# Kernel optimization log

Hardware: AMD Instinct MI355X
Metric: run time of the kernel (lower is better)

Reference implementation:

```python
import jax, jax.numpy as jnp
import numpy as np

EMBED_DIM = 1024
LAMBDA_INIT = 0.8
EPS = 1e-5


def setup_inputs() -> dict:
    key = jax.random.key(0)
    ks = jax.random.split(key, 8)
    D = EMBED_DIM
    x = jax.random.normal(ks[0], (4, 2048, D), dtype=jnp.float32)
    # torch Linear weight [out, in]; we store transposed [in, out] for x @ W
    s = 1.0 / np.sqrt(D)
    w_q12 = jax.random.uniform(ks[1], (D, 2 * D), jnp.float32, -s, s)
    w_k12 = jax.random.uniform(ks[2], (D, 2 * D), jnp.float32, -s, s)
    w_v = jax.random.uniform(ks[3], (D, D), jnp.float32, -s, s)
    lambda_q1 = 0.1 * jax.random.normal(ks[4], (D,), jnp.float32)
    lambda_k1 = 0.1 * jax.random.normal(ks[5], (D,), jnp.float32)
    lambda_q2 = 0.1 * jax.random.normal(ks[6], (D,), jnp.float32)
    lambda_k2 = 0.1 * jax.random.normal(ks[7], (D,), jnp.float32)
    return {"x": x, "w_q12": w_q12, "w_k12": w_k12, "w_v": w_v,
            "lambda_q1": lambda_q1, "lambda_k1": lambda_k1,
            "lambda_q2": lambda_q2, "lambda_k2": lambda_k2}


def reference(x, w_q12, w_k12, w_v, lambda_q1, lambda_k1, lambda_q2, lambda_k2):
    D = x.shape[-1]
    scale = D ** (-0.25)
    q12 = jnp.einsum('bsd,de->bse', x, w_q12)
    k12 = jnp.einsum('bsd,de->bse', x, w_k12)
    q1, q2 = jnp.split(q12, 2, axis=-1)
    k1, k2 = jnp.split(k12, 2, axis=-1)
    v = jnp.einsum('bsd,de->bse', x, w_v)
    attn1 = jnp.einsum('bqd,bkd->bqk', q1, k1) * scale
    attn2 = jnp.einsum('bqd,bkd->bqk', q2, k2) * scale
    lam1 = jnp.exp(jnp.sum(lambda_q1 * lambda_k1))
    lam2 = jnp.exp(jnp.sum(lambda_q2 * lambda_k2))
    lam_full = lam1 - lam2 + LAMBDA_INIT
    diff = jax.nn.softmax(attn1, axis=-1) - lam_full * jax.nn.softmax(attn2, axis=-1)
    out = jnp.einsum('bqk,bkd->bqd', diff, v)
    # RMSNorm (no affine), then scale by (1 - lambda_init)
    rms = jnp.sqrt(jnp.mean(out * out, axis=-1, keepdims=True) + EPS)
    return (out / rms) * (1.0 - LAMBDA_INIT)
```

## Files before the change

kernel.cpp:

```cpp
#include <hip/hip_runtime.h>

typedef float f32x4 __attribute__((ext_vector_type(4)));
typedef _Float16 h16x8 __attribute__((ext_vector_type(8)));
typedef _Float16 h16x4 __attribute__((ext_vector_type(4)));

#define GLOAD_LDS16(gp, lp) __builtin_amdgcn_global_load_lds(               \
    (const __attribute__((address_space(1))) void*)(gp),                    \
    (__attribute__((address_space(3))) void*)(lp), 16, 0, 0)

#define BARX do { __builtin_amdgcn_s_barrier(); asm volatile("" ::: "memory"); } while (0)
#define VMW(N) asm volatile("s_waitcnt vmcnt(" #N ")" ::: "memory")

__global__ __launch_bounds__(256) void cast_x(const float* __restrict__ x,
                                              _Float16* __restrict__ xh) {
  long i = (long)blockIdx.x * 256 + threadIdx.x;
  f32x4 a = *(const f32x4*)(x + i * 8);
  f32x4 b = *(const f32x4*)(x + i * 8 + 4);
  h16x8 h;
  h[0] = (_Float16)a[0]; h[1] = (_Float16)a[1];
  h[2] = (_Float16)a[2]; h[3] = (_Float16)a[3];
  h[4] = (_Float16)b[0]; h[5] = (_Float16)b[1];
  h[6] = (_Float16)b[2]; h[7] = (_Float16)b[3];
  *(h16x8*)(xh + i * 8) = h;
}

__global__ __launch_bounds__(256) void tcw(const float* __restrict__ in,
                                           _Float16* __restrict__ out,
                                           int Kd, int Nd, float scale) {
  __shared__ float tile[64][65];
  const int t = threadIdx.x;
  const int k0 = blockIdx.y * 64, n0 = blockIdx.x * 64;
  const int tr = t >> 4, tc = (t & 15) * 4;
#pragma unroll
  for (int i = 0; i < 4; ++i) {
    int r = i * 16 + tr;
    f32x4 a = *(const f32x4*)(in + (long)(k0 + r) * Nd + n0 + tc);
    tile[r][tc + 0] = a[0]; tile[r][tc + 1] = a[1];
    tile[r][tc + 2] = a[2]; tile[r][tc + 3] = a[3];
  }
  __syncthreads();
#pragma unroll
  for (int i = 0; i < 4; ++i) {
    int r = i * 16 + tr;
    h16x4 h;
#pragma unroll
    for (int q = 0; q < 4; ++q) h[q] = (_Float16)(tile[tc + q][r] * scale);
    *(h16x4*)(out + (long)(n0 + r) * Kd + k0 + tc) = h;
  }
}

__global__ __launch_bounds__(256) void trans16(const _Float16* __restrict__ in,
                                               _Float16* __restrict__ out,
                                               int R, int Cd, long ibatch, long obatch) {
  __shared__ _Float16 tile[64][72];
  in += (long)blockIdx.z * ibatch;
  out += (long)blockIdx.z * obatch;
  const int t = threadIdx.x;
  const int r0 = blockIdx.y * 64, c0 = blockIdx.x * 64;
  const int tr = t >> 3, tc8 = (t & 7) * 8;
#pragma unroll
  for (int i = 0; i < 2; ++i) {
    int r = i * 32 + tr;
    h16x8 a = *(const h16x8*)(in + (long)(r0 + r) * Cd + c0 + tc8);
    *(h16x8*)(&tile[r][tc8]) = a;
  }
  __syncthreads();
#pragma unroll
  for (int i = 0; i < 2; ++i) {
    int r = i * 32 + tr;
    h16x8 h;
#pragma unroll
    for (int q = 0; q < 8; ++q) h[q] = tile[tc8 + q][r];
    *(h16x8*)(out + (long)(c0 + r) * R + r0 + tc8) = h;
  }
}

__global__ __launch_bounds__(1024) void lambda_k(const float* __restrict__ lq1,
                                                 const float* __restrict__ lk1,
                                                 const float* __restrict__ lq2,
                                                 const float* __restrict__ lk2,
                                                 float* __restrict__ lam) {
  __shared__ float sh1[16], sh2[16];
  const int t = threadIdx.x;
  float p1 = lq1[t] * lk1[t];
  float p2 = lq2[t] * lk2[t];
#pragma unroll
  for (int off = 1; off < 64; off <<= 1) {
    p1 += __shfl_xor(p1, off);
    p2 += __shfl_xor(p2, off);
  }
  if ((t & 63) == 0) { sh1[t >> 6] = p1; sh2[t >> 6] = p2; }
  __syncthreads();
  if (t == 0) {
    float s1 = 0.f, s2 = 0.f;
    for (int i = 0; i < 16; ++i) { s1 += sh1[i]; s2 += sh2[i]; }
    lam[0] = __expf(s1) - __expf(s2) + 0.8f;
  }
}

template <typename CT>
__global__ __launch_bounds__(256, 2) void gemmv(
    const _Float16* __restrict__ A, const _Float16* __restrict__ B,
    CT* __restrict__ C, int K, int lda, int ldb, int ldc,
    long abatch, long bbatch, long cbatch, long a2, long c2, int natt,
    int nbx, int nby) {
  __shared__ _Float16 As[3][256 * 32];
  __shared__ _Float16 Bs[3][128 * 32];

  const int nwg = gridDim.x;
  const int orig = blockIdx.x;
  const int qd = nwg >> 3, rm = nwg & 7;
  const int xcd = orig & 7, sub = orig >> 3;
  const int wgid = (xcd < rm ? xcd * (qd + 1) : rm * (qd + 1) + (xcd - rm) * qd) + sub;

  const int z = wgid / (nbx * nby);
  const int rem = wgid - z * nbx * nby;
  const int by = rem / nbx;
  const int bx = rem - by * nbx;
  const int att = z % natt;
  const int bz = z / natt;

  const int t = threadIdx.x;
  const int lane = t & 63, wv = t >> 6;
  const int wm = wv >> 1, wn = wv & 1;
  const int lg = lane >> 4, l15 = lane & 15;

  const _Float16* Ab = A + (long)bz * abatch + (long)att * a2 + (long)(by * 256) * lda;
  const _Float16* Bb = B + (long)bz * bbatch + (long)att * a2 + (long)(bx * 128) * ldb;

  auto stage = [&](int slot, int S) {
    const long ko = (long)S * 32;
#pragma unroll
    for (int j = 0; j < 4; ++j) {
      const int e = t + j * 256;
      const int r = e >> 2;
      const int gs = ((e & 3) - (r >> 1)) & 3;
      GLOAD_LDS16(Ab + (long)r * lda + ko + gs * 8, &As[slot][e * 8]);
    }
#pragma unroll
    for (int j = 0; j < 2; ++j) {
      const int e = t + j * 256;
      const int r = e >> 2;
      const int gs = ((e & 3) - (r >> 1)) & 3;
      GLOAD_LDS16(Bb + (long)r * ldb + ko + gs * 8, &Bs[slot][e * 8]);
    }
  };

  int offA[8], offB[4];
#pragma unroll
  for (int m = 0; m < 8; ++m) {
    const int r = wm * 128 + m * 16 + l15;
    offA[m] = (r * 4 + ((lg + (r >> 1)) & 3)) * 8;
  }
#pragma unroll
  for (int n = 0; n < 4; ++n) {
    const int r = wn * 64 + n * 16 + l15;
    offB[n] = (r * 4 + ((lg + (r >> 1)) & 3)) * 8;
  }

  f32x4 acc[8][4] = {};
  const int NS = K >> 5;

  stage(0, 0); stage(1, 1);
  int cur = 0, nx2 = 2;

  for (int S = 0; S < NS; ++S) {
    if (S == NS - 1) VMW(0);
    else VMW(6);
    BARX;

    if (S + 2 < NS) stage(nx2, S + 2);

    const _Float16* Ap = &As[cur][0];
    const _Float16* Bp = &Bs[cur][0];
    h16x8 a[8], b[4];
#pragma unroll
    for (int m = 0; m < 8; ++m) a[m] = *(const h16x8*)(Ap + offA[m]);
#pragma unroll
    for (int n = 0; n < 4; ++n) b[n] = *(const h16x8*)(Bp + offB[n]);
    __builtin_amdgcn_s_setprio(1);
#pragma unroll
    for (int m = 0; m < 8; ++m)
#pragma unroll
      for (int n = 0; n < 4; ++n)
        acc[m][n] = __builtin_amdgcn_mfma_f32_16x16x32_f16(a[m], b[n], acc[m][n], 0, 0, 0);
    __builtin_amdgcn_s_setprio(0);

    cur = (cur == 2) ? 0 : cur + 1;
    nx2 = (nx2 == 2) ? 0 : nx2 + 1;
  }

  CT* Cb = C + (long)bz * cbatch + (long)att * c2;
  const int crow0 = by * 256 + wm * 128;
  const int ccol0 = bx * 128 + wn * 64;
#pragma unroll
  for (int m = 0; m < 8; ++m)
#pragma unroll
    for (int n = 0; n < 4; ++n)
#pragma unroll
      for (int j = 0; j < 4; ++j)
        Cb[(long)(crow0 + m * 16 + lg * 4 + j) * ldc + ccol0 + n * 16 + l15] =
            (CT)acc[m][n][j];
}

__global__ __launch_bounds__(256) void softmax_diff(const _Float16* __restrict__ S1,
                                                    const _Float16* __restrict__ S2,
                                                    _Float16* __restrict__ D,
                                                    const float* __restrict__ lamp) {
  const long row = (long)blockIdx.x * 4 + (threadIdx.x >> 6);
  const int lane = threadIdx.x & 63;
  const float lam = *lamp;
  const _Float16* s1 = S1 + row * 2048;
  const _Float16* s2 = S2 + row * 2048;
  float v1[32], v2[32];
  float m1 = -3e38f, m2 = -3e38f;
#pragma unroll
  for (int j = 0; j < 4; ++j) {
    h16x8 a = ((const h16x8*)s1)[j * 64 + lane];
    h16x8 b = ((const h16x8*)s2)[j * 64 + lane];
#pragma unroll
    for (int q = 0; q < 8; ++q) {
      v1[j * 8 + q] = (float)a[q]; v2[j * 8 + q] = (float)b[q];
      m1 = fmaxf(m1, v1[j * 8 + q]); m2 = fmaxf(m2, v2[j * 8 + q]);
    }
  }
#pragma unroll
  for (int off = 1; off < 64; off <<= 1) {
    m1 = fmaxf(m1, __shfl_xor(m1, off));
    m2 = fmaxf(m2, __shfl_xor(m2, off));
  }
  float l1 = 0.f, l2 = 0.f;
#pragma unroll
  for (int e = 0; e < 32; ++e) {
    v1[e] = __expf(v1[e] - m1); l1 += v1[e];
    v2[e] = __expf(v2[e] - m2); l2 += v2[e];
  }
#pragma unroll
  for (int off = 1; off < 64; off <<= 1) {
    l1 += __shfl_xor(l1, off);
    l2 += __shfl_xor(l2, off);
  }
  const float r1 = 1.f / l1, r2 = lam / l2;
  _Float16* d = D + row * 2048;
#pragma unroll
  for (int j = 0; j < 4; ++j) {
    h16x8 h;
#pragma unroll
    for (int q = 0; q < 8; ++q)
      h[q] = (_Float16)(v1[j * 8 + q] * r1 - v2[j * 8 + q] * r2);
    ((h16x8*)d)[j * 64 + lane] = h;
  }
}

__global__ __launch_bounds__(256) void rmsnorm(const _Float16* __restrict__ O,
                                               float* __restrict__ out) {
  const long row = (long)blockIdx.x * 4 + (threadIdx.x >> 6);
  const int lane = threadIdx.x & 63;
  const _Float16* o = O + row * 1024;
  h16x8 a = ((const h16x8*)o)[lane];
  h16x8 b = ((const h16x8*)o)[64 + lane];
  float xa[8], xb[8];
  float ss = 0.f;
#pragma unroll
  for (int q = 0; q < 8; ++q) {
    xa[q] = (float)a[q]; xb[q] = (float)b[q];
    ss += xa[q] * xa[q] + xb[q] * xb[q];
  }
#pragma unroll
  for (int off = 1; off < 64; off <<= 1) ss += __shfl_xor(ss, off);
  const float s = 0.2f * rsqrtf(ss * (1.f / 1024.f) + 1e-5f);
  float* po = out + row * 1024;
  f32x4 r;
#pragma unroll
  for (int q = 0; q < 4; ++q) r[q] = xa[q] * s;
  *(f32x4*)(po + lane * 8) = r;
#pragma unroll
  for (int q = 0; q < 4; ++q) r[q] = xa[4 + q] * s;
  *(f32x4*)(po + lane * 8 + 4) = r;
#pragma unroll
  for (int q = 0; q < 4; ++q) r[q] = xb[q] * s;
  *(f32x4*)(po + 512 + lane * 8) = r;
#pragma unroll
  for (int q = 0; q < 4; ++q) r[q] = xb[4 + q] * s;
  *(f32x4*)(po + 512 + lane * 8 + 4) = r;
}

extern "C" void kernel_launch(void* const* d_in, const int* in_sizes, int n_in,
                              void* d_out, int out_size, void* d_ws, size_t ws_size,
                              hipStream_t stream) {
  const float* x   = (const float*)d_in[0];
  const float* wq  = (const float*)d_in[1];
  const float* wk  = (const float*)d_in[2];
  const float* wv  = (const float*)d_in[3];
  const float* lq1 = (const float*)d_in[4];
  const float* lk1 = (const float*)d_in[5];
  const float* lq2 = (const float*)d_in[6];
  const float* lk2 = (const float*)d_in[7];
  float* out = (float*)d_out;

  const size_t MB = 1ull << 20;
  char* ws = (char*)d_ws;
  _Float16* xh   = (_Float16*)(ws + 0);
  _Float16* Wp   = (_Float16*)(ws + 16 * MB);
  _Float16* qkv  = (_Float16*)(ws + 26 * MB);
  _Float16* vt   = (_Float16*)(ws + 106 * MB);
  _Float16* S1   = (_Float16*)(ws + 122 * MB);
  _Float16* S2   = (_Float16*)(ws + 154 * MB);
  float*    lam  = (float*)(ws + 186 * MB);
  _Float16* diff = (_Float16*)(ws + 26 * MB);
  _Float16* opre = (_Float16*)(ws + 58 * MB);

  const float scale = 0.17677669529663689f;

  cast_x<<<4096, 256, 0, stream>>>(x, xh);
  tcw<<<dim3(32, 16), 256, 0, stream>>>(wq, Wp, 1024, 2048, scale);
  tcw<<<dim3(32, 16), 256, 0, stream>>>(wk, Wp + 2048l * 1024, 1024, 2048, 1.0f);
  tcw<<<dim3(16, 16), 256, 0, stream>>>(wv, Wp + 4096l * 1024, 1024, 1024, 1.0f);
  lambda_k<<<1, 1024, 0, stream>>>(lq1, lk1, lq2, lk2, lam);

  gemmv<_Float16><<<1280, 256, 0, stream>>>(xh, Wp, qkv, 1024, 1024, 1024, 5120,
                                            0, 0, 0, 0, 0, 1, 40, 32);

  trans16<<<dim3(16, 32, 4), 256, 0, stream>>>(qkv + 4096, vt, 2048, 5120,
                                               2048l * 5120, 1024l * 2048);

  gemmv<_Float16><<<1024, 256, 0, stream>>>(qkv, qkv + 2048, S1, 1024, 5120, 5120, 2048,
                                            2048l * 5120, 2048l * 5120, 2048l * 2048,
                                            1024, 16777216l, 2, 16, 8);

  softmax_diff<<<2048, 256, 0, stream>>>(S1, S2, diff, lam);

  gemmv<_Float16><<<256, 256, 0, stream>>>(diff, vt, opre, 2048, 2048, 2048, 1024,
                                           2048l * 2048, 1024l * 2048, 2048l * 1024,
                                           0, 0, 1, 8, 8);

  rmsnorm<<<2048, 256, 0, stream>>>(opre, out);
}
```

Measured before the change: 312.8 us.

## Replace GEMM with 8-wave 256x256 tile kernel using ping-pong sub-tile schedule

Replaces the 4-wave 256x128 triple-buffered GEMM with an 8-wave kernel using 256x256 (or 256x128) tiles, K-step 64, and double-buffered half-tiles. The loop interleaves LDS fragment reads, async global-to-LDS loads and four MFMA quadrants separated by barriers, and uses an XOR swizzle. It aims to raise arithmetic intensity per workgroup and hide load latency behind MFMA work. In exchange it adds many barriers and a higher register load, and it halves the grid for the QKV and score GEMMs, which may lower occupancy.

```diff
diff --git a/kernel.cpp b/kernel.cpp
--- a/kernel.cpp
+++ b/kernel.cpp
@@ -98,20 +98,23 @@
   }
 }
 
-template <typename CT>
-__global__ __launch_bounds__(256, 2) void gemmv(
+template <int NREP, typename CT>
+__global__ __launch_bounds__(512, 2) void g8(
     const _Float16* __restrict__ A, const _Float16* __restrict__ B,
     CT* __restrict__ C, int K, int lda, int ldb, int ldc,
     long abatch, long bbatch, long cbatch, long a2, long c2, int natt,
     int nbx, int nby) {
-  __shared__ _Float16 As[3][256 * 32];
-  __shared__ _Float16 Bs[3][128 * 32];
+  constexpr int BN = NREP * 64;
+  constexpr int BNH = BN / 2;
+  constexpr int NH = NREP / 2;
+  __shared__ _Float16 As[2][2][128 * 64];
+  __shared__ _Float16 Bs[2][2][BNH * 64];
 
   const int nwg = gridDim.x;
   const int orig = blockIdx.x;
   const int qd = nwg >> 3, rm = nwg & 7;
-  const int xcd = orig & 7, sub = orig >> 3;
-  const int wgid = (xcd < rm ? xcd * (qd + 1) : rm * (qd + 1) + (xcd - rm) * qd) + sub;
+  const int xcd = orig & 7, sub_ = orig >> 3;
+  const int wgid = (xcd < rm ? xcd * (qd + 1) : rm * (qd + 1) + (xcd - rm) * qd) + sub_;
 
   const int z = wgid / (nbx * nby);
   const int rem = wgid - z * nbx * nby;
@@ -122,85 +125,133 @@
 
   const int t = threadIdx.x;
   const int lane = t & 63, wv = t >> 6;
-  const int wm = wv >> 1, wn = wv & 1;
+  const int wm = wv >> 2, wn = wv & 3;
   const int lg = lane >> 4, l15 = lane & 15;
 
   const _Float16* Ab = A + (long)bz * abatch + (long)att * a2 + (long)(by * 256) * lda;
-  const _Float16* Bb = B + (long)bz * bbatch + (long)att * a2 + (long)(bx * 128) * ldb;
-
-  auto stage = [&](int slot, int S) {
-    const long ko = (long)S * 32;
+  const _Float16* Bb = B + (long)bz * bbatch + (long)att * a2 + (long)(bx * BN) * ldb;
+
+  auto stgA = [&](int T, int s) {
+    const int db = T & 1;
+#pragma unroll
+    for (int j = 0; j < 2; ++j) {
+      const int c = t + j * 512;
+      const int ru = c >> 3, p = c & 7;
+      const int gs = p ^ (ru & 7);
+      const int grow = (ru < 64) ? (s * 64 + ru) : (128 + s * 64 + (ru - 64));
+      GLOAD_LDS16(Ab + (long)grow * lda + T * 64 + gs * 8, &As[db][s][c * 8]);
+    }
+  };
+  auto stgB = [&](int T, int s) {
+    const int db = T & 1;
+#pragma unroll
+    for (int j = 0; j < (NREP == 4 ? 2 : 1); ++j) {
+      const int c = t + j * 512;
+      const int ru = c >> 3, p = c & 7;
+      const int gs = p ^ (ru & 7);
+      GLOAD_LDS16(Bb + (long)(s * BNH + ru) * ldb + T * 64 + gs * 8, &Bs[db][s][c * 8]);
+    }
+  };
+
+  int swz[2];
+  swz[0] = ((lg) ^ (l15 & 7)) * 16;
+  swz[1] = ((4 + lg) ^ (l15 & 7)) * 16;
+
+  h16x8 fA[4][2], fB0[NH][2], fB1[NH][2];
+  f32x4 acc[8][NREP] = {};
+
+  auto rdA = [&](int db, int s) {
+    const char* base = (const char*)&As[db][s][0] + (wm * 64 + l15) * 128;
 #pragma unroll
     for (int j = 0; j < 4; ++j) {
-      const int e = t + j * 256;
-      const int r = e >> 2;
-      const int gs = ((e & 3) - (r >> 1)) & 3;
-      GLOAD_LDS16(Ab + (long)r * lda + ko + gs * 8, &As[slot][e * 8]);
-    }
-#pragma unroll
-    for (int j = 0; j < 2; ++j) {
-      const int e = t + j * 256;
-      const int r = e >> 2;
-      const int gs = ((e & 3) - (r >> 1)) & 3;
-      GLOAD_LDS16(Bb + (long)r * ldb + ko + gs * 8, &Bs[slot][e * 8]);
-    }
-  };
-
-  int offA[8], offB[4];
-#pragma unroll
-  for (int m = 0; m < 8; ++m) {
-    const int r = wm * 128 + m * 16 + l15;
-    offA[m] = (r * 4 + ((lg + (r >> 1)) & 3)) * 8;
-  }
-#pragma unroll
-  for (int n = 0; n < 4; ++n) {
-    const int r = wn * 64 + n * 16 + l15;
-    offB[n] = (r * 4 + ((lg + (r >> 1)) & 3)) * 8;
-  }
-
-  f32x4 acc[8][4] = {};
-  const int NS = K >> 5;
-
-  stage(0, 0); stage(1, 1);
-  int cur = 0, nx2 = 2;
-
-  for (int S = 0; S < NS; ++S) {
-    if (S == NS - 1) VMW(0);
-    else VMW(6);
-    BARX;
-
-    if (S + 2 < NS) stage(nx2, S + 2);
-
-    const _Float16* Ap = &As[cur][0];
-    const _Float16* Bp = &Bs[cur][0];
-    h16x8 a[8], b[4];
-#pragma unroll
-    for (int m = 0; m < 8; ++m) a[m] = *(const h16x8*)(Ap + offA[m]);
-#pragma unroll
-    for (int n = 0; n < 4; ++n) b[n] = *(const h16x8*)(Bp + offB[n]);
+      fA[j][0] = *(const h16x8*)(base + j * 2048 + swz[0]);
+      fA[j][1] = *(const h16x8*)(base + j * 2048 + swz[1]);
+    }
+  };
+  auto rdB = [&](int db, int s, h16x8 (&dst)[NH][2]) {
+    const char* base = (const char*)&Bs[db][s][0] + (wn * (BNH / 4) + l15) * 128;
+#pragma unroll
+    for (int j = 0; j < NH; ++j) {
+      dst[j][0] = *(const h16x8*)(base + j * 2048 + swz[0]);
+      dst[j][1] = *(const h16x8*)(base + j * 2048 + swz[1]);
+    }
+  };
+  auto QUAD = [&](int ms, int ns, h16x8 (&fb)[NH][2]) {
     __builtin_amdgcn_s_setprio(1);
 #pragma unroll
-    for (int m = 0; m < 8; ++m)
-#pragma unroll
-      for (int n = 0; n < 4; ++n)
-        acc[m][n] = __builtin_amdgcn_mfma_f32_16x16x32_f16(a[m], b[n], acc[m][n], 0, 0, 0);
+    for (int j = 0; j < 4; ++j)
+#pragma unroll
+      for (int n = 0; n < NH; ++n) {
+        acc[ms * 4 + j][ns * NH + n] = __builtin_amdgcn_mfma_f32_16x16x32_f16(
+            fA[j][0], fb[n][0], acc[ms * 4 + j][ns * NH + n], 0, 0, 0);
+        acc[ms * 4 + j][ns * NH + n] = __builtin_amdgcn_mfma_f32_16x16x32_f16(
+            fA[j][1], fb[n][1], acc[ms * 4 + j][ns * NH + n], 0, 0, 0);
+      }
     __builtin_amdgcn_s_setprio(0);
-
-    cur = (cur == 2) ? 0 : cur + 1;
-    nx2 = (nx2 == 2) ? 0 : nx2 + 1;
+  };
+
+  const int NT = K >> 6;
+
+  stgB(0, 0); stgA(0, 0); stgB(0, 1); stgA(0, 1); stgB(1, 0); stgA(1, 0); stgB(1, 1);
+  if constexpr (NREP == 4) VMW(6); else VMW(4);
+  BARX;
+
+  for (int T = 0; T + 2 < NT; T += 2) {
+    rdA(0, 0); rdB(0, 0, fB0); stgA(T + 1, 1);
+    BARX; QUAD(0, 0, fB0); BARX;
+    rdB(0, 1, fB1); stgB(T + 2, 0);
+    BARX; QUAD(0, 1, fB1); BARX;
+    rdA(0, 1); stgA(T + 2, 0);
+    BARX; QUAD(1, 1, fB1); BARX;
+    stgB(T + 2, 1);
+    if constexpr (NREP == 4) VMW(6); else VMW(4);
+    BARX; QUAD(1, 0, fB0); BARX;
+    rdA(1, 0); rdB(1, 0, fB0); stgA(T + 2, 1);
+    BARX; QUAD(0, 0, fB0); BARX;
+    rdB(1, 1, fB1); stgB(T + 3, 0);
+    BARX; QUAD(0, 1, fB1); BARX;
+    rdA(1, 1); stgA(T + 3, 0);
+    BARX; QUAD(1, 1, fB1); BARX;
+    stgB(T + 3, 1);
+    if constexpr (NREP == 4) VMW(6); else VMW(4);
+    BARX; QUAD(1, 0, fB0); BARX;
+  }
+
+  {
+    rdA(0, 0); rdB(0, 0, fB0); stgA(NT - 1, 1);
+    BARX; QUAD(0, 0, fB0); BARX;
+    rdB(0, 1, fB1);
+    BARX; QUAD(0, 1, fB1); BARX;
+    rdA(0, 1);
+    BARX; QUAD(1, 1, fB1); BARX;
+    VMW(0);
+    BARX; QUAD(1, 0, fB0); BARX;
+    rdA(1, 0); rdB(1, 0, fB0);
+    BARX; QUAD(0, 0, fB0); BARX;
+    rdB(1, 1, fB1);
+    BARX; QUAD(0, 1, fB1); BARX;
+    rdA(1, 1);
+    BARX; QUAD(1, 1, fB1); BARX;
+    QUAD(1, 0, fB0);
   }
 
   CT* Cb = C + (long)bz * cbatch + (long)att * c2;
   const int crow0 = by * 256 + wm * 128;
-  const int ccol0 = bx * 128 + wn * 64;
-#pragma unroll
-  for (int m = 0; m < 8; ++m)
-#pragma unroll
-    for (int n = 0; n < 4; ++n)
-#pragma unroll
-      for (int j = 0; j < 4; ++j)
-        Cb[(long)(crow0 + m * 16 + lg * 4 + j) * ldc + ccol0 + n * 16 + l15] =
-            (CT)acc[m][n][j];
+  const int ccol0 = bx * BN + wn * (BNH / 4);
+#pragma unroll
+  for (int ms = 0; ms < 2; ++ms)
+#pragma unroll
+    for (int j = 0; j < 4; ++j)
+#pragma unroll
+      for (int ns = 0; ns < 2; ++ns)
+#pragma unroll
+        for (int n = 0; n < NH; ++n)
+#pragma unroll
+          for (int q = 0; q < 4; ++q) {
+            const int row = crow0 + ms * 64 + j * 16 + lg * 4 + q;
+            const int col = ccol0 + ns * BNH + n * 16 + l15;
+            Cb[(long)row * ldc + col] = (CT)acc[ms * 4 + j][ns * NH + n][q];
+          }
 }
 
 __global__ __launch_bounds__(256) void softmax_diff(const _Float16* __restrict__ S1,
@@ -318,19 +369,19 @@
   tcw<<<dim3(16, 16), 256, 0, stream>>>(wv, Wp + 4096l * 1024, 1024, 1024, 1.0f);
   lambda_k<<<1, 1024, 0, stream>>>(lq1, lk1, lq2, lk2, lam);
 
-  gemmv<_Float16><<<1280, 256, 0, stream>>>(xh, Wp, qkv, 1024, 1024, 1024, 5120,
-                                            0, 0, 0, 0, 0, 1, 40, 32);
+  g8<4, _Float16><<<640, 512, 0, stream>>>(xh, Wp, qkv, 1024, 1024, 1024, 5120,
+                                           0, 0, 0, 0, 0, 1, 20, 32);
 
   trans16<<<dim3(16, 32, 4), 256, 0, stream>>>(qkv + 4096, vt, 2048, 5120,
                                                2048l * 5120, 1024l * 2048);
 
-  gemmv<_Float16><<<1024, 256, 0, stream>>>(qkv, qkv + 2048, S1, 1024, 5120, 5120, 2048,
-                                            2048l * 5120, 2048l * 5120, 2048l * 2048,
-                                            1024, 16777216l, 2, 16, 8);
+  g8<4, _Float16><<<512, 512, 0, stream>>>(qkv, qkv + 2048, S1, 1024, 5120, 5120, 2048,
+                                           2048l * 5120, 2048l * 5120, 2048l * 2048,
+                                           1024, 16777216l, 2, 8, 8);
 
   softmax_diff<<<2048, 256, 0, stream>>>(S1, S2, diff, lam);
 
-  gemmv<_Float16><<<256, 256, 0, stream>>>(diff, vt, opre, 2048, 2048, 2048, 1024,
+  g8<2, _Float16><<<256, 512, 0, stream>>>(diff, vt, opre, 2048, 2048, 2048, 1024,
                                            2048l * 2048, 1024l * 2048, 2048l * 1024,
                                            0, 0, 1, 8, 8);
 
```

Measured after the change: 271.7 us, median of 2. -13.1%, faster.
